# Performance work log

Measured on AMD Instinct MI355X. Metric: run time of the kernel, lower is better.

The kernel has to match this reference:

```python
import jax, jax.numpy as jnp
import numpy as np

B, S, D, H, DFF = 2, 2048, 1024, 16, 4096
DK = D // H
EPS = 1e-6
MASK_FILL = -1.0  # original code uses -1**9 == -1 (precedence bug), NOT -1e9


def layernorm(x, gamma, beta):
    # original: (x - mean) / (std + eps), std unbiased (torch default ddof=1), scalar gamma/beta
    mean = jnp.mean(x, axis=-1, keepdims=True)
    std = jnp.std(x, axis=-1, keepdims=True, ddof=1)
    return gamma * (x - mean) / (std + EPS) + beta


def setup_inputs() -> dict:
    key = jax.random.key(0)
    ks = jax.random.split(key, 12)
    sc = 0.02
    return {
        "x": jax.random.normal(ks[0], (B, S, D), jnp.float32),
        "src_mask": jnp.ones((B, 1, 1, S), jnp.int32),
        "wq": jax.random.normal(ks[1], (D, D), jnp.float32) * sc,
        "bq": jnp.zeros((D,), jnp.float32),
        "wk": jax.random.normal(ks[2], (D, D), jnp.float32) * sc,
        "bk": jnp.zeros((D,), jnp.float32),
        "wv": jax.random.normal(ks[3], (D, D), jnp.float32) * sc,
        "bv": jnp.zeros((D,), jnp.float32),
        "wo": jax.random.normal(ks[4], (D, D), jnp.float32) * sc,
        "bo": jnp.zeros((D,), jnp.float32),
        "w1": jax.random.normal(ks[5], (D, DFF), jnp.float32) * sc,
        "b1": jnp.zeros((DFF,), jnp.float32),
        "w2": jax.random.normal(ks[6], (DFF, D), jnp.float32) * sc,
        "b2": jnp.zeros((D,), jnp.float32),
        "g1": jnp.ones((), jnp.float32),
        "be1": jnp.zeros((), jnp.float32),
        "g2": jnp.ones((), jnp.float32),
        "be2": jnp.zeros((), jnp.float32),
    }


def reference(x, src_mask, wq, bq, wk, bk, wv, bv, wo, bo,
              w1, b1, w2, b2, g1, be1, g2, be2):
    # --- residual 1: pre-LN self-attention ---
    xn = layernorm(x, g1, be1)
    q = (xn @ wq + bq).reshape(B, S, H, DK).transpose(0, 2, 1, 3)  # [B,H,S,DK]
    k = (xn @ wk + bk).reshape(B, S, H, DK).transpose(0, 2, 1, 3)
    v = (xn @ wv + bv).reshape(B, S, H, DK).transpose(0, 2, 1, 3)
    scores = jnp.einsum('bhqd,bhkd->bhqk', q, k) / jnp.sqrt(jnp.float32(DK))
    scores = jnp.where(src_mask == 0, MASK_FILL, scores)
    attn = jax.nn.softmax(scores, axis=-1)
    ctx = jnp.einsum('bhqk,bhkd->bhqd', attn, v)
    ctx = ctx.transpose(0, 2, 1, 3).reshape(B, S, D)
    attn_out = ctx @ wo + bo
    x = x + attn_out  # dropout is identity in eval

    # --- residual 2: pre-LN feed-forward ---
    xn = layernorm(x, g2, be2)
    h = jax.nn.relu(xn @ w1 + b1)
    ff_out = h @ w2 + b2
    return x + ff_out
```

## Files before the change

kernel.cpp:

```cpp
#include <hip/hip_runtime.h>

typedef unsigned short u16;
typedef __bf16 bf16x8 __attribute__((ext_vector_type(8)));
typedef float f32x4 __attribute__((ext_vector_type(4)));
typedef float f32x16 __attribute__((ext_vector_type(16)));

#define AS1U(p) ((__attribute__((address_space(1))) unsigned int*)(p))
#define AS3U(p) ((__attribute__((address_space(3))) unsigned int*)(p))

__device__ __forceinline__ u16 f2bf(float f) {
  union { float f; unsigned int i; } c; c.f = f;
  return (u16)((c.i + 0x7FFFu + ((c.i >> 16) & 1u)) >> 16);
}
__device__ __forceinline__ u16 f2bf_trunc(float f) {
  union { float f; unsigned int i; } c; c.f = f;
  return (u16)(c.i >> 16);
}
__device__ __forceinline__ unsigned cvt_pk_bf16(float lo, float hi) {
  unsigned r;
  asm("v_cvt_pk_bf16_f32 %0, %1, %2" : "=v"(r) : "v"(lo), "v"(hi));
  return r;
}
__device__ __forceinline__ void plswap(unsigned& a, unsigned& b) {
  asm("v_permlane32_swap_b32 %0, %1" : "+v"(a), "+v"(b));
}

template <int OMODE>
__global__ __launch_bounds__(512, 2) void gemm3(
    const u16* __restrict__ A, long lda,
    const u16* __restrict__ B, long ldb,
    void* __restrict__ Cv, long ldc,
    int K, const float* __restrict__ bias,
    const float* __restrict__ res, long ldres, int relu) {
  __shared__ u16 As[3][256 * 64];
  __shared__ u16 Bs[3][128 * 64];
  const int t = threadIdx.x;
  const int w = t >> 6, l = t & 63;
  const int hi = l >> 5, lq = l & 31;
  const int wm = w >> 1, wn = w & 1;
  const long row0 = (long)blockIdx.x * 256;
  const long col0 = (long)blockIdx.y * 128;

  auto stage = [&](int slot, int k0) {
#pragma unroll
    for (int i = 0; i < 4; i++) {
      int s = t + i * 512, r = s >> 3, c = s & 7;
      __builtin_amdgcn_global_load_lds(AS1U(A + (row0 + r) * lda + k0 + (c ^ (r & 7)) * 8),
                                       AS3U(&As[slot][s * 8]), 16, 0, 0);
    }
#pragma unroll
    for (int i = 0; i < 2; i++) {
      int s = t + i * 512, r = s >> 3, c = s & 7;
      __builtin_amdgcn_global_load_lds(AS1U(B + (col0 + r) * ldb + k0 + (c ^ (r & 7)) * 8),
                                       AS3U(&Bs[slot][s * 8]), 16, 0, 0);
    }
  };

  f32x16 acc[2][2] = {};
  const int NT = K >> 6;

  stage(0, 0);
  stage(1, 64);
  asm volatile("s_waitcnt vmcnt(6)" ::: "memory");
  __builtin_amdgcn_s_barrier();
  __builtin_amdgcn_sched_barrier(0);

  int s0 = 0, s1 = 1, s2 = 2;
  for (int kt = 0; kt < NT; kt++) {
    if (kt + 2 < NT) stage(s2, (kt + 2) * 64);
    bf16x8 a[2][4], b[2][4];
#pragma unroll
    for (int mi = 0; mi < 2; mi++) {
      const int r = wm * 64 + mi * 32 + lq;
#pragma unroll
      for (int kk = 0; kk < 4; kk++)
        a[mi][kk] = *(const bf16x8*)&As[s0][(r * 8 + ((kk * 2 + hi) ^ (r & 7))) * 8];
    }
#pragma unroll
    for (int nj = 0; nj < 2; nj++) {
      const int r = wn * 64 + nj * 32 + lq;
#pragma unroll
      for (int kk = 0; kk < 4; kk++)
        b[nj][kk] = *(const bf16x8*)&Bs[s0][(r * 8 + ((kk * 2 + hi) ^ (r & 7))) * 8];
    }
    __builtin_amdgcn_s_setprio(1);
#pragma unroll
    for (int kk = 0; kk < 4; kk++)
#pragma unroll
      for (int mi = 0; mi < 2; mi++)
#pragma unroll
        for (int nj = 0; nj < 2; nj++)
          acc[mi][nj] = __builtin_amdgcn_mfma_f32_32x32x16_bf16(a[mi][kk], b[nj][kk], acc[mi][nj], 0, 0, 0);
    __builtin_amdgcn_s_setprio(0);
    if (kt + 2 < NT) {
      asm volatile("s_waitcnt vmcnt(6)" ::: "memory");
    } else {
      asm volatile("s_waitcnt vmcnt(0)" ::: "memory");
    }
    __builtin_amdgcn_s_barrier();
    __builtin_amdgcn_sched_barrier(0);
    const int tmp = s0; s0 = s1; s1 = s2; s2 = tmp;
  }

#pragma unroll
  for (int nj = 0; nj < 2; nj++) {
    const long gn = col0 + wn * 64 + nj * 32 + lq;
    const float bv = bias ? bias[gn] : 0.0f;
#pragma unroll
    for (int mi = 0; mi < 2; mi++) {
#pragma unroll
      for (int g = 0; g < 16; g++) {
        const long gm = row0 + wm * 64 + mi * 32 + (g & 3) + 8 * (g >> 2) + 4 * hi;
        float v = acc[mi][nj][g] + bv;
        if (relu && v < 0.0f) v = 0.0f;
        if (res) v += res[gm * ldres + gn];
        if (OMODE == 0) ((float*)Cv)[gm * ldc + gn] = v;
        else ((u16*)Cv)[gm * ldc + gn] = f2bf(v);
      }
    }
  }
}

template <int BM, int BN, int BK, int OMODE>
__global__ __launch_bounds__(256) void gemm_bt(
    const u16* __restrict__ A, long lda,
    const u16* __restrict__ B, long ldb,
    void* __restrict__ Cv, long ldc,
    int K, float scale, const float* __restrict__ bias,
    const float* __restrict__ res, long ldres, int relu) {
  constexpr int WN = (BN == 128) ? 64 : 32;
  constexpr int MI = 4, NJ = WN / 16;
  constexpr int KK = BK / 32;
  __shared__ u16 As0[BM * BK], As1[BM * BK];
  __shared__ u16 Bs0[BN * BK], Bs1[BN * BK];
  const int t = threadIdx.x;
  const int w = t >> 6, l = t & 63;
  const int wr = w >> 1, wc = w & 1;
  const int quad = l >> 4, mlo = l & 15;
  const long row0 = (long)blockIdx.x * BM;
  const long col0 = (long)blockIdx.y * BN;

  f32x4 acc[MI][NJ] = {};

  auto stage = [&](u16 (&Ad)[BM * BK], u16 (&Bd)[BN * BK], int k0) {
    if (BK == 32) {
#pragma unroll
      for (int i = 0; i < BM / 64; i++) {
        int s = t + i * 256, r = s >> 2, c = s & 3;
        const u16* g = A + (row0 + r) * lda + k0 + c * 8;
        __builtin_amdgcn_global_load_lds(AS1U(g), AS3U(&Ad[s * 8]), 16, 0, 0);
      }
#pragma unroll
      for (int i = 0; i < BN / 64; i++) {
        int s = t + i * 256, r = s >> 2, c = s & 3;
        const u16* g = B + (col0 + r) * ldb + k0 + c * 8;
        __builtin_amdgcn_global_load_lds(AS1U(g), AS3U(&Bd[s * 8]), 16, 0, 0);
      }
    } else {
#pragma unroll
      for (int i = 0; i < BM / 32; i++) {
        int s = t + i * 256, r = s >> 3, c = s & 7;
        const u16* g = A + (row0 + r) * lda + k0 + (c ^ (r & 7)) * 8;
        __builtin_amdgcn_global_load_lds(AS1U(g), AS3U(&Ad[s * 8]), 16, 0, 0);
      }
#pragma unroll
      for (int i = 0; i < BN / 32; i++) {
        int s = t + i * 256, r = s >> 3, c = s & 7;
        const u16* g = B + (col0 + r) * ldb + k0 + (c ^ (r & 7)) * 8;
        __builtin_amdgcn_global_load_lds(AS1U(g), AS3U(&Bd[s * 8]), 16, 0, 0);
      }
    }
  };
  auto compute = [&](const u16 (&Asr)[BM * BK], const u16 (&Bsr)[BN * BK]) {
#pragma unroll
    for (int kk = 0; kk < KK; kk++) {
      bf16x8 a[MI], b[NJ];
#pragma unroll
      for (int i = 0; i < MI; i++) {
        int r = wr * 64 + i * 16 + mlo;
        a[i] = (BK == 32) ? *(const bf16x8*)&Asr[(r * 4 + quad) * 8]
                          : *(const bf16x8*)&Asr[(r * 8 + ((kk * 4 + quad) ^ (r & 7))) * 8];
      }
#pragma unroll
      for (int j = 0; j < NJ; j++) {
        int r = wc * WN + j * 16 + mlo;
        b[j] = (BK == 32) ? *(const bf16x8*)&Bsr[(r * 4 + quad) * 8]
                          : *(const bf16x8*)&Bsr[(r * 8 + ((kk * 4 + quad) ^ (r & 7))) * 8];
      }
#pragma unroll
      for (int i = 0; i < MI; i++)
#pragma unroll
        for (int j = 0; j < NJ; j++)
          acc[i][j] = __builtin_amdgcn_mfma_f32_16x16x32_bf16(a[i], b[j], acc[i][j], 0, 0, 0);
    }
  };

  stage(As0, Bs0, 0);
  for (int k0 = 0; k0 < K; k0 += 2 * BK) {
    __syncthreads();
    stage(As1, Bs1, k0 + BK);
    compute(As0, Bs0);
    __syncthreads();
    if (k0 + 2 * BK < K) stage(As0, Bs0, k0 + 2 * BK);
    compute(As1, Bs1);
  }

#pragma unroll
  for (int i = 0; i < MI; i++) {
#pragma unroll
    for (int j = 0; j < NJ; j++) {
      const long gn = col0 + wc * WN + j * 16 + mlo;
      const float bv = bias ? bias[gn] : 0.0f;
#pragma unroll
      for (int r = 0; r < 4; r++) {
        const long gm = row0 + wr * 64 + i * 16 + quad * 4 + r;
        float v = acc[i][j][r] * scale + bv;
        if (relu && v < 0.0f) v = 0.0f;
        if (res) v += res[gm * ldres + gn];
        if (OMODE == 0) ((float*)Cv)[gm * ldc + gn] = v;
        else ((u16*)Cv)[gm * ldc + gn] = f2bf(v);
      }
    }
  }
}

__global__ __launch_bounds__(256, 2) void flash_attn(
    const u16* __restrict__ QKV, const u16* __restrict__ VT,
    const int* __restrict__ mask, u16* __restrict__ ctx) {
  __shared__ u16 Ks[2][64 * 64];
  __shared__ u16 Vs[2][64 * 64];
  const int t = threadIdx.x;
  const int w = t >> 6, l = t & 63;
  const int hi = l >> 5, lq = l & 31, rx = lq & 7;
  const int z = blockIdx.z, b = z >> 4, h = z & 15;
  const long q0 = (long)blockIdx.x * 128;
  const u16* Qg = QKV + (long)b * (2048L * 3072) + h * 64;
  const u16* Kg = Qg + 1024;
  const u16* Vg = VT + (long)b * (1024L * 2048) + (long)(h * 64) * 2048;
  const int* mrow = mask + b * 2048;

#pragma unroll
  for (int i = 0; i < 2; i++) {
    int s = t + i * 256, r = s >> 3, c = s & 7;
    __builtin_amdgcn_global_load_lds(AS1U(Kg + (long)r * 3072 + (c ^ (r & 7)) * 8),
                                     AS3U(&Ks[0][s * 8]), 16, 0, 0);
    __builtin_amdgcn_global_load_lds(AS1U(Vg + (long)r * 2048 + (c ^ (r & 7)) * 8),
                                     AS3U(&Vs[0][s * 8]), 16, 0, 0);
  }

  const float CS = 0.125f * 1.44269504f;
  const float CM = -1.44269504f;

  bf16x8 aq[4];
#pragma unroll
  for (int kk = 0; kk < 4; kk++) {
    const u16* g = Qg + (q0 + w * 32 + lq) * 3072 + kk * 16 + hi * 8;
    union { uint4 u; bf16x8 v; u16 s[8]; } cc; cc.u = *(const uint4*)g;
#pragma unroll
    for (int e = 0; e < 8; e++) {
      union { unsigned u; float f; } qf; qf.u = (unsigned)cc.s[e] << 16;
      cc.s[e] = f2bf(qf.f * CS);
    }
    aq[kk] = cc.v;
  }

  unsigned am = 0;
  for (int it = 0; it < 32; ++it) {
    unsigned long long bmv = __ballot(mrow[it * 64 + l] != 0);
    am |= ((bmv == ~0ull) ? 1u : 0u) << it;
  }

  f32x16 o[2] = {}, den = {};
  union { u16 s[8]; bf16x8 v; } ones;
#pragma unroll
  for (int e = 0; e < 8; e++) ones.s[e] = 0x3F80;

  for (int it = 0; it < 32; ++it) {
    const int cur = it & 1;
    __syncthreads();
    if (it + 1 < 32) {
      const int nb = 1 - cur;
      const u16* Kg2 = Kg + (long)(it + 1) * 64 * 3072;
      const u16* Vg2 = Vg + (it + 1) * 64;
#pragma unroll
      for (int i2 = 0; i2 < 2; i2++) {
        int s = t + i2 * 256, r = s >> 3, c = s & 7;
        __builtin_amdgcn_global_load_lds(AS1U(Kg2 + (long)r * 3072 + (c ^ (r & 7)) * 8),
                                         AS3U(&Ks[nb][s * 8]), 16, 0, 0);
        __builtin_amdgcn_global_load_lds(AS1U(Vg2 + (long)r * 2048 + (c ^ (r & 7)) * 8),
                                         AS3U(&Vs[nb][s * 8]), 16, 0, 0);
      }
    }
    const bool allone = (am >> it) & 1u;
    unsigned long long bm = ~0ull;
    if (!allone) bm = __ballot(mrow[it * 64 + l] != 0);

    f32x16 sa[2];
    __builtin_amdgcn_s_setprio(1);
#pragma unroll
    for (int kt = 0; kt < 2; kt++) {
      f32x16 s0 = {};
      const int rk = kt * 32 + lq;
#pragma unroll
      for (int kk = 0; kk < 4; kk++) {
        bf16x8 ak = *(const bf16x8*)&Ks[cur][(rk * 8 + ((2 * kk + hi) ^ rx)) * 8];
        s0 = __builtin_amdgcn_mfma_f32_32x32x16_bf16(ak, aq[kk], s0, 0, 0, 0);
      }
      sa[kt] = s0;
    }
    __builtin_amdgcn_s_setprio(0);

#pragma unroll
    for (int kt = 0; kt < 2; kt++) {
      float p[16];
      if (allone) {
#pragma unroll
        for (int g = 0; g < 16; g++) p[g] = __builtin_amdgcn_exp2f(sa[kt][g]);
      } else {
#pragma unroll
        for (int g = 0; g < 16; g++) {
          const int k = kt * 32 + (g & 3) + 8 * (g >> 2) + 4 * hi;
          const float s = ((bm >> k) & 1) ? sa[kt][g] : CM;
          p[g] = __builtin_amdgcn_exp2f(s);
        }
      }
      unsigned wd[4][2];
#pragma unroll
      for (int g = 0; g < 4; g++) {
        wd[g][0] = cvt_pk_bf16(p[4 * g + 0], p[4 * g + 1]);
        wd[g][1] = cvt_pk_bf16(p[4 * g + 2], p[4 * g + 3]);
      }
#pragma unroll
      for (int c = 0; c < 2; c++) {
        plswap(wd[2 * c][0], wd[2 * c + 1][0]);
        plswap(wd[2 * c][1], wd[2 * c + 1][1]);
        union { unsigned u[4]; bf16x8 v; } pa;
        pa.u[0] = wd[2 * c][0];
        pa.u[1] = wd[2 * c][1];
        pa.u[2] = wd[2 * c + 1][0];
        pa.u[3] = wd[2 * c + 1][1];
        const int cg = kt * 2 + c;
        __builtin_amdgcn_s_setprio(1);
#pragma unroll
        for (int dt = 0; dt < 2; dt++) {
          const int rv = dt * 32 + lq;
          bf16x8 bv = *(const bf16x8*)&Vs[cur][(rv * 8 + ((2 * cg + hi) ^ rx)) * 8];
          o[dt] = __builtin_amdgcn_mfma_f32_32x32x16_bf16(pa.v, bv, o[dt], 0, 0, 0);
        }
        den = __builtin_amdgcn_mfma_f32_32x32x16_bf16(pa.v, ones.v, den, 0, 0, 0);
        __builtin_amdgcn_s_setprio(0);
      }
    }
  }

  u16* cb = ctx + (long)b * (2048L * 1024) + (q0 + w * 32) * 1024 + h * 64;
#pragma unroll
  for (int g = 0; g < 16; g++) {
    const int row = (g & 3) + 8 * (g >> 2) + 4 * hi;
    const float inv = 1.0f / den[g];
    cb[(long)row * 1024 + lq] = f2bf(o[0][g] * inv);
    cb[(long)row * 1024 + 32 + lq] = f2bf(o[1][g] * inv);
  }
}

__device__ __forceinline__ void ln_row(const float* __restrict__ x, u16* __restrict__ y,
                                       const float* __restrict__ g, const float* __restrict__ b,
                                       long row, float* ss, float* s2) {
  const float* xr = x + row * 1024;
  float v[4];
  float s = 0.f, sq = 0.f;
#pragma unroll
  for (int i = 0; i < 4; i++) {
    float f = xr[threadIdx.x + i * 256];
    v[i] = f; s += f; sq += f * f;
  }
#pragma unroll
  for (int o = 32; o > 0; o >>= 1) { s += __shfl_xor(s, o, 64); sq += __shfl_xor(sq, o, 64); }
  const int w = threadIdx.x >> 6;
  if ((threadIdx.x & 63) == 0) { ss[w] = s; s2[w] = sq; }
  __syncthreads();
  s = ss[0] + ss[1] + ss[2] + ss[3];
  sq = s2[0] + s2[1] + s2[2] + s2[3];
  const float mean = s * (1.0f / 1024.0f);
  float var = (sq - s * mean) * (1.0f / 1023.0f);
  var = fmaxf(var, 0.0f);
  const float sc = g[0] / (sqrtf(var) + 1e-6f);
  const float be = b[0];
#pragma unroll
  for (int i = 0; i < 4; i++)
    y[row * 1024 + threadIdx.x + i * 256] = f2bf((v[i] - mean) * sc + be);
}

__global__ __launch_bounds__(256) void ln_kernel(const float* __restrict__ x, u16* __restrict__ y,
                                                 const float* __restrict__ g, const float* __restrict__ b) {
  __shared__ float ss[4], s2[4];
  ln_row(x, y, g, b, blockIdx.x, ss, s2);
}

__global__ __launch_bounds__(256) void prep_kernel(
    const float* __restrict__ x, const float* __restrict__ g1, const float* __restrict__ be1,
    const float* __restrict__ wq, const float* __restrict__ wk, const float* __restrict__ wv,
    const float* __restrict__ wo, const float* __restrict__ w1, const float* __restrict__ w2,
    const float* __restrict__ bq, const float* __restrict__ bk, const float* __restrict__ bv,
    u16* __restrict__ xnH, u16* __restrict__ WqkvT, u16* __restrict__ woT,
    u16* __restrict__ w1T, u16* __restrict__ w2T, float* __restrict__ biasQKV) {
  __shared__ float tile[32][33];
  __shared__ float ss[4], s2[4];
  const int bid = blockIdx.x;
  if (bid >= 12300) {
    ln_row(x, xnH, g1, be1, bid - 12300, ss, s2);
    return;
  }
  if (bid >= 12288) {
    const int i = (bid - 12288) * 256 + threadIdx.x;
    if (i < 3072) biasQKV[i] = (i < 1024) ? bq[i] : ((i < 2048) ? bk[i - 1024] : bv[i - 2048]);
    return;
  }
  const float* in; u16* out; long ldin, ldo; int ti, tiles_x;
  if (bid < 1024)      { in = wq; out = WqkvT;                     ldin = 1024; ldo = 1024; ti = bid;        tiles_x = 32; }
  else if (bid < 2048) { in = wk; out = WqkvT + (size_t)1024*1024; ldin = 1024; ldo = 1024; ti = bid - 1024; tiles_x = 32; }
  else if (bid < 3072) { in = wv; out = WqkvT + (size_t)2048*1024; ldin = 1024; ldo = 1024; ti = bid - 2048; tiles_x = 32; }
  else if (bid < 4096) { in = wo; out = woT;                       ldin = 1024; ldo = 1024; ti = bid - 3072; tiles_x = 32; }
  else if (bid < 8192) { in = w1; out = w1T;                       ldin = 4096; ldo = 1024; ti = bid - 4096; tiles_x = 128; }
  else                 { in = w2; out = w2T;                       ldin = 1024; ldo = 4096; ti = bid - 8192; tiles_x = 32; }
  const int bx = (ti % tiles_x) * 32, by = (ti / tiles_x) * 32;
  const int tx = threadIdx.x & 31, ty = threadIdx.x >> 5;
#pragma unroll
  for (int i = 0; i < 32; i += 8) tile[ty + i][tx] = in[(long)(by + ty + i) * ldin + bx + tx];
  __syncthreads();
#pragma unroll
  for (int i = 0; i < 32; i += 8)
    out[(long)(bx + ty + i) * ldo + by + tx] = f2bf(tile[tx][ty + i]);
}

__global__ __launch_bounds__(256) void ttrans1(const u16* __restrict__ in, long ldin, long siz,
                                               u16* __restrict__ out, long ldo, long soz) {
  __shared__ u16 tile[32][33];
  const long zi = (long)blockIdx.z * siz, zo = (long)blockIdx.z * soz;
  const int bx = blockIdx.x * 32, by = blockIdx.y * 32;
  const int tx = threadIdx.x & 31, ty = threadIdx.x >> 5;
#pragma unroll
  for (int i = 0; i < 32; i += 8)
    tile[ty + i][tx] = in[zi + (long)(by + ty + i) * ldin + bx + tx];
  __syncthreads();
#pragma unroll
  for (int i = 0; i < 32; i += 8)
    out[zo + (long)(bx + ty + i) * ldo + by + tx] = tile[tx][ty + i];
}

extern "C" void kernel_launch(void* const* d_in, const int* in_sizes, int n_in,
                              void* d_out, int out_size, void* d_ws, size_t ws_size,
                              hipStream_t stream) {
  const float* x   = (const float*)d_in[0];
  const int*   msk = (const int*)d_in[1];
  const float* wq  = (const float*)d_in[2];
  const float* bq  = (const float*)d_in[3];
  const float* wk  = (const float*)d_in[4];
  const float* bk  = (const float*)d_in[5];
  const float* wv  = (const float*)d_in[6];
  const float* bv  = (const float*)d_in[7];
  const float* wo  = (const float*)d_in[8];
  const float* bo  = (const float*)d_in[9];
  const float* w1  = (const float*)d_in[10];
  const float* b1  = (const float*)d_in[11];
  const float* w2  = (const float*)d_in[12];
  const float* b2  = (const float*)d_in[13];
  const float* g1  = (const float*)d_in[14];
  const float* be1 = (const float*)d_in[15];
  const float* g2  = (const float*)d_in[16];
  const float* be2 = (const float*)d_in[17];
  float* out = (float*)d_out;

  char* basep = (char*)d_ws;
  size_t off = 0;
  auto au = [&](size_t nelem) -> u16* {
    u16* r = (u16*)(basep + off);
    off += ((nelem * 2) + 255) & ~(size_t)255;
    return r;
  };
  auto afp = [&](size_t nelem) -> float* {
    float* r = (float*)(basep + off);
    off += ((nelem * 4) + 255) & ~(size_t)255;
    return r;
  };

  u16* xnH  = au((size_t)4096 * 1024);
  u16* QKV  = au((size_t)4096 * 3072);
  u16* VTH  = au((size_t)2 * 1024 * 2048);
  u16* ctxH = au((size_t)4096 * 1024);
  float* x1 = afp((size_t)4096 * 1024);
  u16* hb   = au((size_t)4096 * 4096);
  u16* WqkvT = au((size_t)3072 * 1024);
  u16* woT  = au((size_t)1024 * 1024);
  u16* w1T  = au((size_t)4096 * 1024);
  u16* w2T  = au((size_t)1024 * 4096);
  float* biasQKV = afp(3072);

  const dim3 blk(256);
  const dim3 blk5(512);

  prep_kernel<<<16396, blk, 0, stream>>>(x, g1, be1, wq, wk, wv, wo, w1, w2,
                                         bq, bk, bv, xnH, WqkvT, woT, w1T, w2T, biasQKV);

  gemm3<2><<<dim3(16, 24), blk5, 0, stream>>>(
      xnH, 1024, WqkvT, 1024, QKV, 3072, 1024,
      biasQKV, (const float*)0, 0, 0);

  ttrans1<<<dim3(32, 64, 2), blk, 0, stream>>>(
      QKV + 2048, 3072, (long)2048 * 3072, VTH, 2048, (long)1024 * 2048);

  flash_attn<<<dim3(16, 1, 32), blk, 0, stream>>>(QKV, VTH, msk, ctxH);

  gemm_bt<128, 64, 64, 0><<<dim3(32, 16), blk, 0, stream>>>(
      ctxH, 1024, woT, 1024, x1, 1024, 1024, 1.0f, bo, x, 1024, 0);

  ln_kernel<<<4096, blk, 0, stream>>>(x1, xnH, g2, be2);

  gemm3<2><<<dim3(16, 32), blk5, 0, stream>>>(
      xnH, 1024, w1T, 1024, hb, 4096, 1024,
      b1, (const float*)0, 0, 1);

  gemm_bt<128, 64, 64, 0><<<dim3(32, 16), blk, 0, stream>>>(
      hb, 4096, w2T, 4096, out, 1024, 4096, 1.0f, b2, x1, 1024, 0);
}
```

Baseline: 365.6 us.

## Replace 256x128 triple-buffered GEMM with 256x256 double-buffered interleaved-staging GEMM

Measured after the change: 343.1 us. 1.07x faster.

```diff
diff --git a/kernel.cpp b/kernel.cpp
--- a/kernel.cpp
+++ b/kernel.cpp
@@ -26,80 +26,90 @@
 }
 
 template <int OMODE>
-__global__ __launch_bounds__(512, 2) void gemm3(
+__global__ __launch_bounds__(512, 2) void gemm8(
     const u16* __restrict__ A, long lda,
     const u16* __restrict__ B, long ldb,
     void* __restrict__ Cv, long ldc,
     int K, const float* __restrict__ bias,
     const float* __restrict__ res, long ldres, int relu) {
-  __shared__ u16 As[3][256 * 64];
-  __shared__ u16 Bs[3][128 * 64];
+  __shared__ u16 As[2][256 * 64];
+  __shared__ u16 Bs[2][256 * 64];
   const int t = threadIdx.x;
   const int w = t >> 6, l = t & 63;
   const int hi = l >> 5, lq = l & 31;
-  const int wm = w >> 1, wn = w & 1;
+  const int wm = w >> 2, wn = w & 3;
   const long row0 = (long)blockIdx.x * 256;
-  const long col0 = (long)blockIdx.y * 128;
-
-  auto stage = [&](int slot, int k0) {
-#pragma unroll
-    for (int i = 0; i < 4; i++) {
-      int s = t + i * 512, r = s >> 3, c = s & 7;
-      __builtin_amdgcn_global_load_lds(AS1U(A + (row0 + r) * lda + k0 + (c ^ (r & 7)) * 8),
-                                       AS3U(&As[slot][s * 8]), 16, 0, 0);
-    }
+  const long col0 = (long)blockIdx.y * 256;
+
+  auto stageU = [&](int bb, int unit, int k0) {
+    const u16* src = (unit < 2) ? B : A;
+    const long ld = (unit < 2) ? ldb : lda;
+    const long base0 = (unit < 2) ? col0 : row0;
+    u16* dst = (unit < 2) ? &Bs[bb][0] : &As[bb][0];
+    const int h = unit & 1;
 #pragma unroll
     for (int i = 0; i < 2; i++) {
-      int s = t + i * 512, r = s >> 3, c = s & 7;
-      __builtin_amdgcn_global_load_lds(AS1U(B + (col0 + r) * ldb + k0 + (c ^ (r & 7)) * 8),
-                                       AS3U(&Bs[slot][s * 8]), 16, 0, 0);
+      int s = t + i * 512;
+      int r = h * 128 + (s >> 3), c = s & 7;
+      __builtin_amdgcn_global_load_lds(AS1U(src + (base0 + r) * ld + k0 + ((c ^ (r & 7)) * 8)),
+                                       AS3U(dst + ((long)(r * 8 + c)) * 8), 16, 0, 0);
     }
   };
 
-  f32x16 acc[2][2] = {};
+  f32x16 acc[4][2] = {};
   const int NT = K >> 6;
 
-  stage(0, 0);
-  stage(1, 64);
-  asm volatile("s_waitcnt vmcnt(6)" ::: "memory");
+  stageU(0, 0, 0); stageU(0, 1, 0); stageU(0, 2, 0); stageU(0, 3, 0);
+  if (NT > 1) stageU(1, 0, 64);
+  asm volatile("s_waitcnt vmcnt(2)" ::: "memory");
+  __builtin_amdgcn_sched_barrier(0);
   __builtin_amdgcn_s_barrier();
   __builtin_amdgcn_sched_barrier(0);
 
-  int s0 = 0, s1 = 1, s2 = 2;
-  for (int kt = 0; kt < NT; kt++) {
-    if (kt + 2 < NT) stage(s2, (kt + 2) * 64);
-    bf16x8 a[2][4], b[2][4];
-#pragma unroll
-    for (int mi = 0; mi < 2; mi++) {
-      const int r = wm * 64 + mi * 32 + lq;
+  bf16x8 bfr[2][4];
+  for (int tt = 0; tt < NT; tt++) {
+    const int cb = tt & 1, nb = cb ^ 1;
+    const int kN = (tt + 1) << 6, kN2 = (tt + 2) << 6;
+#pragma unroll
+    for (int mi = 0; mi < 4; mi++) {
+      bf16x8 afr[4];
+      {
+        const int r = wm * 128 + mi * 32 + lq;
+#pragma unroll
+        for (int kk = 0; kk < 4; kk++)
+          afr[kk] = *(const bf16x8*)&As[cb][(r * 8 + ((kk * 2 + hi) ^ (r & 7))) * 8];
+      }
+      if (mi == 0) {
+#pragma unroll
+        for (int nj = 0; nj < 2; nj++) {
+          const int r = wn * 64 + nj * 32 + lq;
+#pragma unroll
+          for (int kk = 0; kk < 4; kk++)
+            bfr[nj][kk] = *(const bf16x8*)&Bs[cb][(r * 8 + ((kk * 2 + hi) ^ (r & 7))) * 8];
+        }
+      }
+      if (mi == 0) { if (tt + 1 < NT) stageU(nb, 1, kN); }
+      else if (mi == 1) { if (tt + 1 < NT) stageU(nb, 2, kN); }
+      else if (mi == 2) { if (tt + 1 < NT) stageU(nb, 3, kN); }
+      else {
+        if (tt + 2 < NT) stageU(cb, 0, kN2);
+        if (tt < NT - 2) asm volatile("s_waitcnt vmcnt(2)" ::: "memory");
+        else             asm volatile("s_waitcnt vmcnt(0)" ::: "memory");
+      }
+      __builtin_amdgcn_sched_barrier(0);
+      __builtin_amdgcn_s_barrier();
+      __builtin_amdgcn_sched_barrier(0);
+      __builtin_amdgcn_s_setprio(1);
 #pragma unroll
       for (int kk = 0; kk < 4; kk++)
-        a[mi][kk] = *(const bf16x8*)&As[s0][(r * 8 + ((kk * 2 + hi) ^ (r & 7))) * 8];
-    }
-#pragma unroll
-    for (int nj = 0; nj < 2; nj++) {
-      const int r = wn * 64 + nj * 32 + lq;
-#pragma unroll
-      for (int kk = 0; kk < 4; kk++)
-        b[nj][kk] = *(const bf16x8*)&Bs[s0][(r * 8 + ((kk * 2 + hi) ^ (r & 7))) * 8];
-    }
-    __builtin_amdgcn_s_setprio(1);
-#pragma unroll
-    for (int kk = 0; kk < 4; kk++)
-#pragma unroll
-      for (int mi = 0; mi < 2; mi++)
 #pragma unroll
         for (int nj = 0; nj < 2; nj++)
-          acc[mi][nj] = __builtin_amdgcn_mfma_f32_32x32x16_bf16(a[mi][kk], b[nj][kk], acc[mi][nj], 0, 0, 0);
-    __builtin_amdgcn_s_setprio(0);
-    if (kt + 2 < NT) {
-      asm volatile("s_waitcnt vmcnt(6)" ::: "memory");
-    } else {
-      asm volatile("s_waitcnt vmcnt(0)" ::: "memory");
-    }
-    __builtin_amdgcn_s_barrier();
-    __builtin_amdgcn_sched_barrier(0);
-    const int tmp = s0; s0 = s1; s1 = s2; s2 = tmp;
+          acc[mi][nj] = __builtin_amdgcn_mfma_f32_32x32x16_bf16(afr[kk], bfr[nj][kk], acc[mi][nj], 0, 0, 0);
+      __builtin_amdgcn_s_setprio(0);
+      __builtin_amdgcn_sched_barrier(0);
+      __builtin_amdgcn_s_barrier();
+      __builtin_amdgcn_sched_barrier(0);
+    }
   }
 
 #pragma unroll
@@ -107,10 +117,10 @@
     const long gn = col0 + wn * 64 + nj * 32 + lq;
     const float bv = bias ? bias[gn] : 0.0f;
 #pragma unroll
-    for (int mi = 0; mi < 2; mi++) {
+    for (int mi = 0; mi < 4; mi++) {
 #pragma unroll
       for (int g = 0; g < 16; g++) {
-        const long gm = row0 + wm * 64 + mi * 32 + (g & 3) + 8 * (g >> 2) + 4 * hi;
+        const long gm = row0 + wm * 128 + mi * 32 + (g & 3) + 8 * (g >> 2) + 4 * hi;
         float v = acc[mi][nj][g] + bv;
         if (relu && v < 0.0f) v = 0.0f;
         if (res) v += res[gm * ldres + gn];
@@ -502,7 +512,7 @@
   prep_kernel<<<16396, blk, 0, stream>>>(x, g1, be1, wq, wk, wv, wo, w1, w2,
                                          bq, bk, bv, xnH, WqkvT, woT, w1T, w2T, biasQKV);
 
-  gemm3<2><<<dim3(16, 24), blk5, 0, stream>>>(
+  gemm8<2><<<dim3(16, 12), blk5, 0, stream>>>(
       xnH, 1024, WqkvT, 1024, QKV, 3072, 1024,
       biasQKV, (const float*)0, 0, 0);
 
@@ -516,7 +526,7 @@
 
   ln_kernel<<<4096, blk, 0, stream>>>(x1, xnH, g2, be2);
 
-  gemm3<2><<<dim3(16, 32), blk5, 0, stream>>>(
+  gemm8<2><<<dim3(16, 16), blk5, 0, stream>>>(
       xnH, 1024, w1T, 1024, hb, 4096, 1024,
       b1, (const float*)0, 0, 1);
 
```
